# Kernel tuning notes

Hardware: AMD Instinct MI355X
Metric: run time of the kernel (lower is better)

## Reference

```python
import jax, jax.numpy as jnp
import numpy as np

B, T, C, H = 2, 2048, 1024, 16
HS = C // H

def setup_inputs() -> dict:
    key = jax.random.key(0)
    ks = jax.random.split(key, 5)
    s = 0.02
    return {
        "x": jax.random.normal(ks[0], (B, T, C), jnp.float32),
        "W_attn": jax.random.normal(ks[1], (C, 3 * C), jnp.float32) * s,
        "b_attn": jax.random.normal(ks[2], (3 * C,), jnp.float32) * s,
        "W_proj": jax.random.normal(ks[3], (C, C), jnp.float32) * s,
        "b_proj": jax.random.normal(ks[4], (C,), jnp.float32) * s,
    }

def reference(x, W_attn, b_attn, W_proj, b_proj):
    qkv = x @ W_attn + b_attn                      # [B,T,3C]
    q, k, v = jnp.split(qkv, 3, axis=-1)
    # [B,T,C] -> [B,H,T,hs]
    def heads(t):
        return t.reshape(B, T, H, HS).transpose(0, 2, 1, 3)
    q, k, v = heads(q), heads(k), heads(v)
    scale = 1.0 / jnp.sqrt(jnp.asarray(HS, x.dtype))
    attn = jnp.einsum('bhqd,bhkd->bhqk', q, k) * scale
    causal = jnp.tril(jnp.ones((T, T), bool))
    attn = jnp.where(causal[None, None], attn, -jnp.inf)
    attn = jax.nn.softmax(attn, axis=-1)
    y = jnp.einsum('bhqk,bhkd->bhqd', attn, v)
    y = y.transpose(0, 2, 1, 3).reshape(B, T, C)
    return y @ W_proj + b_proj
```

## Files before the change

### kernel.cpp

```cpp
#include <hip/hip_runtime.h>
#include <hip/hip_bf16.h>

static constexpr int Bn = 2, Tn = 2048, Cn = 1024, Hn = 16, HSn = 64;
static constexpr int Mrows = Bn * Tn;
static constexpr size_t PL = (size_t)Bn * Hn * Tn * HSn;

typedef __attribute__((ext_vector_type(8))) short short8;
typedef __attribute__((ext_vector_type(4))) float f32x4;

__device__ __forceinline__ unsigned short f2bf(float f) {
  __hip_bfloat16 h = __float2bfloat16(f);
  return *reinterpret_cast<unsigned short*>(&h);
}

__device__ __forceinline__ float fexp2(float x) {
  return __builtin_amdgcn_exp2f(x);
}

__device__ __forceinline__ void gload_lds16(const void* g, void* l) {
  __builtin_amdgcn_global_load_lds(
      (const __attribute__((address_space(1))) void*)g,
      (__attribute__((address_space(3))) void*)l, 16, 0, 0);
}

#define QSC 0.18033688011112042591999058512524f

__global__ __launch_bounds__(256) void prep_all(
    const float* __restrict__ x, unsigned short* __restrict__ xb,
    const float* __restrict__ Wa, unsigned short* __restrict__ Wab,
    const float* __restrict__ Wp, unsigned short* __restrict__ Wpb)
{
  const int bid = blockIdx.x, tid = threadIdx.x;
  if (bid < 4096) {
    int i = bid * 256 + tid;
    float4 v = ((const float4*)x)[i];
    ushort4 o;
    o.x = f2bf(v.x); o.y = f2bf(v.y); o.z = f2bf(v.z); o.w = f2bf(v.w);
    ((ushort4*)xb)[i] = o;
    return;
  }
  __shared__ float tile[32][33];
  const float* src; unsigned short* dst; int R, Cc, tb;
  if (bid < 4096 + 3072) { src = Wa; dst = Wab; R = Cn; Cc = 3 * Cn; tb = bid - 4096; }
  else                   { src = Wp; dst = Wpb; R = Cn; Cc = Cn;     tb = bid - 4096 - 3072; }
  const int nbx = Cc / 32;
  const int bx = tb % nbx, by = tb / nbx;
  const int tx = tid & 31, ty = tid >> 5;
  const int c0 = bx * 32, r0 = by * 32;
  #pragma unroll
  for (int i = 0; i < 4; ++i)
    tile[ty + 8 * i][tx] = src[(size_t)(r0 + ty + 8 * i) * Cc + c0 + tx];
  __syncthreads();
  #pragma unroll
  for (int i = 0; i < 4; ++i)
    dst[(size_t)(c0 + ty + 8 * i) * R + r0 + tx] = f2bf(tile[tx][ty + 8 * i]);
}

__global__ __launch_bounds__(512) void gemmQKV(
    const unsigned short* __restrict__ A, const unsigned short* __restrict__ Bt,
    const float* __restrict__ bias, unsigned short* __restrict__ qkv, int K)
{
  constexpr int NSTEP = 1024 / 64;
  constexpr int AF = 32;
  constexpr int BF = 24;
  __shared__ alignas(16) unsigned char lds[2][(AF + BF) * 1024];

  const int tid = threadIdx.x, wave = tid >> 6, lane = tid & 63;
  const int wr = wave >> 2, wc = wave & 3;
  const int orig = blockIdx.x;
  const int swz = (orig & 7) * 32 + (orig >> 3);
  const int bx = swz & 15, by = swz >> 4;
  const int tM = by * 256, tN = bx * 192;

  auto STAGE = [&](int buf, int k0) {
    #pragma unroll
    for (int i = 0; i < 7; ++i) {
      int f = wave * 7 + i;
      const unsigned short* g;
      int off;
      if (f < AF) {
        int mg = f >> 1, ks = f & 1;
        g = A + (size_t)(tM + mg * 16 + (lane & 15)) * K + k0 + ks * 32 + (lane >> 4) * 8;
        off = f * 1024;
      } else {
        int fg = f - AF;
        int ng = fg >> 1, ks = fg & 1;
        g = Bt + (size_t)(tN + ng * 16 + (lane & 15)) * K + k0 + ks * 32 + (lane >> 4) * 8;
        off = AF * 1024 + fg * 1024;
      }
      gload_lds16(g, &lds[buf][off]);
    }
  };

  f32x4 acc[8][3] = {};

  STAGE(0, 0);
  STAGE(1, 64);

  for (int t = 0; t < NSTEP; ++t) {
    if (t == NSTEP - 1)
      asm volatile("s_waitcnt vmcnt(0)" ::: "memory");
    else
      asm volatile("s_waitcnt vmcnt(7)" ::: "memory");
    __builtin_amdgcn_s_barrier();

    const int cur = t & 1;
    short8 af[8][2], bfr[3][2];
    #pragma unroll
    for (int ks = 0; ks < 2; ++ks) {
      #pragma unroll
      for (int m = 0; m < 8; ++m)
        af[m][ks] = *(const short8*)&lds[cur][((wr * 8 + m) * 2 + ks) * 1024 + lane * 16];
      #pragma unroll
      for (int n = 0; n < 3; ++n)
        bfr[n][ks] = *(const short8*)&lds[cur][AF * 1024 + ((wc * 3 + n) * 2 + ks) * 1024 + lane * 16];
    }
    asm volatile("s_waitcnt lgkmcnt(0)" ::: "memory");
    __builtin_amdgcn_sched_barrier(0);
    __builtin_amdgcn_s_barrier();

    if (t + 2 < NSTEP) STAGE(cur, (t + 2) * 64);

    __builtin_amdgcn_s_setprio(1);
    #pragma unroll
    for (int ks = 0; ks < 2; ++ks)
      #pragma unroll
      for (int m = 0; m < 8; ++m)
        #pragma unroll
        for (int n = 0; n < 3; ++n)
          acc[m][n] = __builtin_amdgcn_mfma_f32_16x16x32_bf16(af[m][ks], bfr[n][ks], acc[m][n], 0, 0, 0);
    __builtin_amdgcn_s_setprio(0);
  }

  const int a = lane & 15, hq = lane >> 4;
  #pragma unroll
  for (int m = 0; m < 8; ++m) {
    #pragma unroll
    for (int n = 0; n < 3; ++n) {
      int c = tN + wc * 48 + n * 16 + a;
      float bv = bias[c];
      int which = c >> 10;
      int cc = c & 1023, hh = cc >> 6, d = cc & 63;
      int row0 = tM + wr * 128 + m * 16 + hq * 4;
      int b = row0 >> 11, t0 = row0 & 2047;
      int bh = b * Hn + hh;
      if (which == 2) {
        ushort4 pk;
        pk.x = f2bf(acc[m][n][0] + bv);
        pk.y = f2bf(acc[m][n][1] + bv);
        pk.z = f2bf(acc[m][n][2] + bv);
        pk.w = f2bf(acc[m][n][3] + bv);
        *(ushort4*)&qkv[2 * PL + ((size_t)bh * HSn + d) * Tn + t0] = pk;
      } else {
        float sc = (which == 0) ? QSC : 1.0f;
        #pragma unroll
        for (int r = 0; r < 4; ++r) {
          float v = (acc[m][n][r] + bv) * sc;
          qkv[(size_t)which * PL + ((size_t)bh * Tn + t0 + r) * HSn + d] = f2bf(v);
        }
      }
    }
  }
}

template <int WM, int WN>
__global__ __launch_bounds__(256) void gemmP(
    const unsigned short* __restrict__ A, const unsigned short* __restrict__ Bt,
    const float* __restrict__ bias, float* __restrict__ O, int N, int K)
{
  constexpr int BM = WM * 32, BNt = WN * 32;
  constexpr int AF = BM / 16;
  constexpr int BF = BNt / 16;
  constexpr int NF = AF + BF;
  constexpr int PW = NF / 4;
  static_assert(PW == 3, "vmcnt literal");
  __shared__ alignas(16) unsigned char lds[2][NF * 1024];

  const int tid = threadIdx.x, wave = tid >> 6, lane = tid & 63;
  const int wr = wave >> 1, wc = wave & 1;
  const int tM = blockIdx.y * BM, tN = blockIdx.x * BNt;

  auto STAGE = [&](int buf, int k0) {
    #pragma unroll
    for (int i = 0; i < PW; ++i) {
      int f = wave * PW + i;
      const unsigned short* g;
      if (f < AF)
        g = A + (size_t)(tM + f * 16 + (lane & 15)) * K + k0 + (lane >> 4) * 8;
      else
        g = Bt + (size_t)(tN + (f - AF) * 16 + (lane & 15)) * K + k0 + (lane >> 4) * 8;
      gload_lds16(g, &lds[buf][f * 1024]);
    }
  };

  f32x4 acc[WM][WN] = {};

  STAGE(0, 0);
  for (int t = 0, k0 = 0;; ++t, k0 += 32) {
    const int cur = t & 1;
    if (k0 + 32 < K) {
      STAGE(cur ^ 1, k0 + 32);
      asm volatile("s_waitcnt vmcnt(3)" ::: "memory");
    } else {
      asm volatile("s_waitcnt vmcnt(0)" ::: "memory");
    }
    __builtin_amdgcn_s_barrier();

    short8 af[WM], bfr[WN];
    #pragma unroll
    for (int m = 0; m < WM; ++m)
      af[m] = *(const short8*)&lds[cur][(wr * WM + m) * 1024 + lane * 16];
    #pragma unroll
    for (int n = 0; n < WN; ++n)
      bfr[n] = *(const short8*)&lds[cur][(AF + wc * WN + n) * 1024 + lane * 16];
    #pragma unroll
    for (int m = 0; m < WM; ++m)
      #pragma unroll
      for (int n = 0; n < WN; ++n)
        acc[m][n] = __builtin_amdgcn_mfma_f32_16x16x32_bf16(af[m], bfr[n], acc[m][n], 0, 0, 0);

    __builtin_amdgcn_s_barrier();
    if (k0 + 32 >= K) break;
  }

  const int a = lane & 15, hq = lane >> 4;
  #pragma unroll
  for (int m = 0; m < WM; ++m) {
    #pragma unroll
    for (int n = 0; n < WN; ++n) {
      int c = tN + wc * (WN * 16) + n * 16 + a;
      float bv = bias[c];
      int r0 = tM + wr * (WM * 16) + m * 16 + hq * 4;
      #pragma unroll
      for (int r = 0; r < 4; ++r)
        O[(size_t)(r0 + r) * N + c] = acc[m][n][r] + bv;
    }
  }
}

__global__ __launch_bounds__(256) void attn_mfma(
    const unsigned short* __restrict__ Qg, const unsigned short* __restrict__ Kg,
    const unsigned short* __restrict__ Vtg, unsigned short* __restrict__ Y)
{
  __shared__ alignas(16) unsigned char lds[50432];
  const int bh = blockIdx.x;
  const int yb = blockIdx.y;
  const int kq = yb >> 3, jq = yb & 7;
  const int qt = kq * 8 + ((kq & 1) ? (7 - jq) : jq);
  const int tid = threadIdx.x, wave = tid >> 6, lane = tid & 63;
  const int a = lane & 15, h = lane >> 4;
  const int a7 = a & 7;
  const int q0 = qt * 64;
  const unsigned short* Qp = Qg + (size_t)bh * Tn * HSn;
  const unsigned short* Kp = Kg + (size_t)bh * Tn * HSn;
  const unsigned short* Vp = Vtg + (size_t)bh * HSn * Tn;
  const int pbase = 40960 + wave * 2368;
  const int qglob = wave * 16 + a;

  #pragma unroll
  for (int i = 0; i < 2; ++i) {
    int r8 = wave * 16 + i * 8;
    int row = r8 + (lane >> 3);
    int ch = (lane & 7) ^ (row & 7);
    gload_lds16(Qp + (size_t)(q0 + row) * HSn + ch * 8, &lds[r8 * 128]);
  }
  __syncthreads();
  short8 qf[2];
  #pragma unroll
  for (int ks = 0; ks < 2; ++ks) {
    int row = wave * 16 + a;
    int ch = (ks * 4 + h) ^ (row & 7);
    qf[ks] = *(const short8*)&lds[row * 128 + ch * 16];
  }

  f32x4 o[4] = {};
  float l = 0.f;

  const int npairs = qt >> 1;
  const bool oddtail = (qt & 1) != 0;
  const int ntotal = npairs + (oddtail ? 1 : 0);

  for (int p = 0; p < ntotal; ++p) {
    const int kv0 = p * 128;
    const bool masked = oddtail && (p == npairs);
    __syncthreads();
    #pragma unroll
    for (int i = 0; i < 4; ++i) {
      int r8 = wave * 32 + i * 8;
      int row = r8 + (lane >> 3);
      int ch = (lane & 7) ^ (row & 7);
      gload_lds16(Kp + (size_t)(kv0 + row) * HSn + ch * 8, &lds[8192 + r8 * 128]);
    }
    #pragma unroll
    for (int i = 0; i < 4; ++i) {
      int d4 = wave * 16 + i * 4;
      int d = d4 + (lane >> 4);
      int ch = (lane & 15) ^ (d & 7);
      gload_lds16(Vp + (size_t)d * Tn + kv0 + ch * 8, &lds[24576 + d4 * 256]);
    }
    __syncthreads();

    f32x4 s[8] = {};
    __builtin_amdgcn_s_setprio(1);
    #pragma unroll
    for (int ks = 0; ks < 2; ++ks)
      #pragma unroll
      for (int n = 0; n < 8; ++n) {
        int kr = n * 16 + a;
        int ch = (ks * 4 + h) ^ a7;
        short8 kf = *(const short8*)&lds[8192 + kr * 128 + ch * 16];
        s[n] = __builtin_amdgcn_mfma_f32_16x16x32_bf16(kf, qf[ks], s[n], 0, 0, 0);
      }
    __builtin_amdgcn_s_setprio(0);

    if (masked) {
      #pragma unroll
      for (int n = 0; n < 8; ++n)
        #pragma unroll
        for (int r = 0; r < 4; ++r)
          if ((kv0 + n * 16 + h * 4 + r) > (q0 + qglob)) s[n][r] = -1e30f;
    }

    float psum = 0.f;
    #pragma unroll
    for (int n = 0; n < 8; ++n)
      #pragma unroll
      for (int r = 0; r < 4; ++r) {
        float ppv = fexp2(s[n][r]);
        s[n][r] = ppv;
        psum += ppv;
      }
    psum += __shfl_xor(psum, 16);
    psum += __shfl_xor(psum, 32);
    l += psum;

    #pragma unroll
    for (int hp = 0; hp < 2; ++hp) {
      #pragma unroll
      for (int nn = 0; nn < 4; ++nn) {
        int n = hp * 4 + nn;
        uint2 w2;
        w2.x = (unsigned)f2bf(s[n][0]) | ((unsigned)f2bf(s[n][1]) << 16);
        w2.y = (unsigned)f2bf(s[n][2]) | ((unsigned)f2bf(s[n][3]) << 16);
        *(uint2*)&lds[pbase + (a * 36 + nn * 8 + h * 2) * 4] = w2;
      }
      __builtin_amdgcn_s_setprio(1);
      #pragma unroll
      for (int ks = 0; ks < 2; ++ks) {
        short8 pa = *(const short8*)&lds[pbase + (a * 36 + ks * 16 + h * 4) * 4];
        #pragma unroll
        for (int n = 0; n < 4; ++n) {
          int d = n * 16 + a;
          int ch = (hp * 8 + ks * 4 + h) ^ a7;
          short8 vf = *(const short8*)&lds[24576 + d * 256 + ch * 16];
          o[n] = __builtin_amdgcn_mfma_f32_16x16x32_bf16(pa, vf, o[n], 0, 0, 0);
        }
      }
      __builtin_amdgcn_s_setprio(0);
    }
  }

  if (!oddtail) {
    const int kv0 = qt * 64;
    __syncthreads();
    #pragma unroll
    for (int i = 0; i < 2; ++i) {
      int r8 = wave * 16 + i * 8;
      int row = r8 + (lane >> 3);
      int ch = (lane & 7) ^ (row & 7);
      gload_lds16(Kp + (size_t)(kv0 + row) * HSn + ch * 8, &lds[8192 + r8 * 128]);
      gload_lds16(Vp + (size_t)row * Tn + kv0 + ch * 8, &lds[24576 + r8 * 128]);
    }
    __syncthreads();

    f32x4 s[4] = {};
    __builtin_amdgcn_s_setprio(1);
    #pragma unroll
    for (int ks = 0; ks < 2; ++ks)
      #pragma unroll
      for (int n = 0; n < 4; ++n) {
        int kr = n * 16 + a;
        int ch = (ks * 4 + h) ^ a7;
        short8 kf = *(const short8*)&lds[8192 + kr * 128 + ch * 16];
        s[n] = __builtin_amdgcn_mfma_f32_16x16x32_bf16(kf, qf[ks], s[n], 0, 0, 0);
      }
    __builtin_amdgcn_s_setprio(0);

    float psum = 0.f;
    #pragma unroll
    for (int n = 0; n < 4; ++n)
      #pragma unroll
      for (int r = 0; r < 4; ++r) {
        float sv = s[n][r];
        if ((n * 16 + h * 4 + r) > qglob) sv = -1e30f;
        float ppv = fexp2(sv);
        s[n][r] = ppv;
        psum += ppv;
      }
    psum += __shfl_xor(psum, 16);
    psum += __shfl_xor(psum, 32);
    l += psum;

    #pragma unroll
    for (int n = 0; n < 4; ++n) {
      uint2 w2;
      w2.x = (unsigned)f2bf(s[n][0]) | ((unsigned)f2bf(s[n][1]) << 16);
      w2.y = (unsigned)f2bf(s[n][2]) | ((unsigned)f2bf(s[n][3]) << 16);
      *(uint2*)&lds[pbase + (a * 36 + n * 8 + h * 2) * 4] = w2;
    }
    __builtin_amdgcn_s_setprio(1);
    #pragma unroll
    for (int ks = 0; ks < 2; ++ks) {
      short8 pa = *(const short8*)&lds[pbase + (a * 36 + ks * 16 + h * 4) * 4];
      #pragma unroll
      for (int n = 0; n < 4; ++n) {
        int d = n * 16 + a;
        int ch = (ks * 4 + h) ^ a7;
        short8 vf = *(const short8*)&lds[24576 + d * 128 + ch * 16];
        o[n] = __builtin_amdgcn_mfma_f32_16x16x32_bf16(pa, vf, o[n], 0, 0, 0);
      }
    }
    __builtin_amdgcn_s_setprio(0);
  }

  if (h == 0) *(float*)&lds[pbase + 2304 + a * 4] = l;
  f32x4 l4 = *(const f32x4*)&lds[pbase + 2304 + h * 16];
  f32x4 inv;
  #pragma unroll
  for (int r = 0; r < 4; ++r) inv[r] = 1.0f / l4[r];
  const int b = bh >> 4, hd = bh & 15;
  #pragma unroll
  for (int n = 0; n < 4; ++n)
    #pragma unroll
    for (int r = 0; r < 4; ++r) {
      int t = q0 + wave * 16 + 4 * h + r;
      int col = hd * 64 + n * 16 + a;
      Y[((size_t)(b * Tn + t)) * Cn + col] = f2bf(o[n][r] * inv[r]);
    }
}

extern "C" void kernel_launch(void* const* d_in, const int* in_sizes, int n_in,
                              void* d_out, int out_size, void* d_ws, size_t ws_size,
                              hipStream_t stream) {
  const float* x      = (const float*)d_in[0];
  const float* W_attn = (const float*)d_in[1];
  const float* b_attn = (const float*)d_in[2];
  const float* W_proj = (const float*)d_in[3];
  const float* b_proj = (const float*)d_in[4];
  float* out = (float*)d_out;

  unsigned short* xb  = (unsigned short*)d_ws;
  unsigned short* Wab = xb + (size_t)Mrows * Cn;
  unsigned short* Wpb = Wab + (size_t)3 * Cn * Cn;
  unsigned short* qkv = Wpb + (size_t)Cn * Cn;
  unsigned short* y   = qkv + 3 * PL;

  prep_all<<<4096 + 3072 + 1024, 256, 0, stream>>>(x, xb, W_attn, Wab, W_proj, Wpb);

  gemmQKV<<<256, 512, 0, stream>>>(xb, Wab, b_attn, qkv, Cn);

  attn_mfma<<<dim3(Bn * Hn, Tn / 64), 256, 0, stream>>>(qkv, qkv + PL, qkv + 2 * PL, y);

  gemmP<4, 2><<<dim3(Cn / 64, Mrows / 128), 256, 0, stream>>>(
      y, Wpb, b_proj, out, Cn, Cn);
}
```

Baseline: 115.3 us.

## Double attention query tile to 128 rows per block and share K/V fragments

Each attention block now covers 128 query rows instead of 64. Each wave computes two 16-row sub-tiles that reuse the same K and V LDS fragments, and the odd/even tail path is replaced by one uniform causal-masked diagonal tile. Softmax row sums now come from an MFMA against a vector of bf16 ones instead of shuffle reductions. The aim is to halve K/V global and LDS traffic per query row and cut per-tile overhead, at the cost of half as many blocks (512), more registers per thread, and an extra barrier per iteration because the P buffer now overlaps the K region.

```diff
diff --git a/kernel.cpp b/kernel.cpp
--- a/kernel.cpp
+++ b/kernel.cpp
@@ -242,65 +242,64 @@
     const unsigned short* __restrict__ Qg, const unsigned short* __restrict__ Kg,
     const unsigned short* __restrict__ Vtg, unsigned short* __restrict__ Y)
 {
-  __shared__ alignas(16) unsigned char lds[50432];
+  __shared__ alignas(16) unsigned char lds[49152];
   const int bh = blockIdx.x;
   const int yb = blockIdx.y;
-  const int kq = yb >> 3, jq = yb & 7;
-  const int qt = kq * 8 + ((kq & 1) ? (7 - jq) : jq);
+  const int qt = (yb < 8) ? yb : 23 - yb;
   const int tid = threadIdx.x, wave = tid >> 6, lane = tid & 63;
   const int a = lane & 15, h = lane >> 4;
   const int a7 = a & 7;
-  const int q0 = qt * 64;
+  const int q0 = qt * 128;
   const unsigned short* Qp = Qg + (size_t)bh * Tn * HSn;
   const unsigned short* Kp = Kg + (size_t)bh * Tn * HSn;
   const unsigned short* Vp = Vtg + (size_t)bh * HSn * Tn;
-  const int pbase = 40960 + wave * 2368;
-  const int qglob = wave * 16 + a;
-
-  #pragma unroll
-  for (int i = 0; i < 2; ++i) {
-    int r8 = wave * 16 + i * 8;
+  const int pbase = wave * 4608;
+
+  #pragma unroll
+  for (int i = 0; i < 4; ++i) {
+    int r8 = wave * 32 + i * 8;
     int row = r8 + (lane >> 3);
     int ch = (lane & 7) ^ (row & 7);
     gload_lds16(Qp + (size_t)(q0 + row) * HSn + ch * 8, &lds[r8 * 128]);
   }
   __syncthreads();
-  short8 qf[2];
+  short8 qfA[2], qfB[2];
   #pragma unroll
   for (int ks = 0; ks < 2; ++ks) {
-    int row = wave * 16 + a;
-    int ch = (ks * 4 + h) ^ (row & 7);
-    qf[ks] = *(const short8*)&lds[row * 128 + ch * 16];
-  }
-
-  f32x4 o[4] = {};
-  float l = 0.f;
-
-  const int npairs = qt >> 1;
-  const bool oddtail = (qt & 1) != 0;
-  const int ntotal = npairs + (oddtail ? 1 : 0);
-
-  for (int p = 0; p < ntotal; ++p) {
+    int rowA = wave * 32 + a;
+    int ch = (ks * 4 + h) ^ (rowA & 7);
+    qfA[ks] = *(const short8*)&lds[rowA * 128 + ch * 16];
+    qfB[ks] = *(const short8*)&lds[(rowA + 16) * 128 + ch * 16];
+  }
+
+  short8 ones;
+  #pragma unroll
+  for (int j = 0; j < 8; ++j) ones[j] = (short)0x3F80;
+
+  f32x4 oA[4] = {}, oB[4] = {};
+  f32x4 lA = {}, lB = {};
+
+  for (int p = 0; p <= qt; ++p) {
     const int kv0 = p * 128;
-    const bool masked = oddtail && (p == npairs);
+    const bool masked = (p == qt);
     __syncthreads();
     #pragma unroll
     for (int i = 0; i < 4; ++i) {
       int r8 = wave * 32 + i * 8;
       int row = r8 + (lane >> 3);
       int ch = (lane & 7) ^ (row & 7);
-      gload_lds16(Kp + (size_t)(kv0 + row) * HSn + ch * 8, &lds[8192 + r8 * 128]);
+      gload_lds16(Kp + (size_t)(kv0 + row) * HSn + ch * 8, &lds[16384 + r8 * 128]);
     }
     #pragma unroll
     for (int i = 0; i < 4; ++i) {
       int d4 = wave * 16 + i * 4;
       int d = d4 + (lane >> 4);
       int ch = (lane & 15) ^ (d & 7);
-      gload_lds16(Vp + (size_t)d * Tn + kv0 + ch * 8, &lds[24576 + d4 * 256]);
+      gload_lds16(Vp + (size_t)d * Tn + kv0 + ch * 8, &lds[32768 + d4 * 256]);
     }
     __syncthreads();
 
-    f32x4 s[8] = {};
+    f32x4 sA[8] = {}, sB[8] = {};
     __builtin_amdgcn_s_setprio(1);
     #pragma unroll
     for (int ks = 0; ks < 2; ++ks)
@@ -308,8 +307,9 @@
       for (int n = 0; n < 8; ++n) {
         int kr = n * 16 + a;
         int ch = (ks * 4 + h) ^ a7;
-        short8 kf = *(const short8*)&lds[8192 + kr * 128 + ch * 16];
-        s[n] = __builtin_amdgcn_mfma_f32_16x16x32_bf16(kf, qf[ks], s[n], 0, 0, 0);
+        short8 kf = *(const short8*)&lds[16384 + kr * 128 + ch * 16];
+        sA[n] = __builtin_amdgcn_mfma_f32_16x16x32_bf16(kf, qfA[ks], sA[n], 0, 0, 0);
+        sB[n] = __builtin_amdgcn_mfma_f32_16x16x32_bf16(kf, qfB[ks], sB[n], 0, 0, 0);
       }
     __builtin_amdgcn_s_setprio(0);
 
@@ -317,22 +317,21 @@
       #pragma unroll
       for (int n = 0; n < 8; ++n)
         #pragma unroll
-        for (int r = 0; r < 4; ++r)
-          if ((kv0 + n * 16 + h * 4 + r) > (q0 + qglob)) s[n][r] = -1e30f;
-    }
-
-    float psum = 0.f;
+        for (int r = 0; r < 4; ++r) {
+          int kv = n * 16 + h * 4 + r;
+          if (kv > (wave * 32 + a)) sA[n][r] = -1e30f;
+          if (kv > (wave * 32 + 16 + a)) sB[n][r] = -1e30f;
+        }
+    }
     #pragma unroll
     for (int n = 0; n < 8; ++n)
       #pragma unroll
       for (int r = 0; r < 4; ++r) {
-        float ppv = fexp2(s[n][r]);
-        s[n][r] = ppv;
-        psum += ppv;
-      }
-    psum += __shfl_xor(psum, 16);
-    psum += __shfl_xor(psum, 32);
-    l += psum;
+        sA[n][r] = fexp2(sA[n][r]);
+        sB[n][r] = fexp2(sB[n][r]);
+      }
+
+    __syncthreads();
 
     #pragma unroll
     for (int hp = 0; hp < 2; ++hp) {
@@ -340,102 +339,49 @@
       for (int nn = 0; nn < 4; ++nn) {
         int n = hp * 4 + nn;
         uint2 w2;
-        w2.x = (unsigned)f2bf(s[n][0]) | ((unsigned)f2bf(s[n][1]) << 16);
-        w2.y = (unsigned)f2bf(s[n][2]) | ((unsigned)f2bf(s[n][3]) << 16);
+        w2.x = (unsigned)f2bf(sA[n][0]) | ((unsigned)f2bf(sA[n][1]) << 16);
+        w2.y = (unsigned)f2bf(sA[n][2]) | ((unsigned)f2bf(sA[n][3]) << 16);
         *(uint2*)&lds[pbase + (a * 36 + nn * 8 + h * 2) * 4] = w2;
+        uint2 v2;
+        v2.x = (unsigned)f2bf(sB[n][0]) | ((unsigned)f2bf(sB[n][1]) << 16);
+        v2.y = (unsigned)f2bf(sB[n][2]) | ((unsigned)f2bf(sB[n][3]) << 16);
+        *(uint2*)&lds[pbase + 2304 + (a * 36 + nn * 8 + h * 2) * 4] = v2;
       }
       __builtin_amdgcn_s_setprio(1);
       #pragma unroll
       for (int ks = 0; ks < 2; ++ks) {
-        short8 pa = *(const short8*)&lds[pbase + (a * 36 + ks * 16 + h * 4) * 4];
+        short8 paA = *(const short8*)&lds[pbase + (a * 36 + ks * 16 + h * 4) * 4];
+        short8 paB = *(const short8*)&lds[pbase + 2304 + (a * 36 + ks * 16 + h * 4) * 4];
+        lA = __builtin_amdgcn_mfma_f32_16x16x32_bf16(paA, ones, lA, 0, 0, 0);
+        lB = __builtin_amdgcn_mfma_f32_16x16x32_bf16(paB, ones, lB, 0, 0, 0);
         #pragma unroll
         for (int n = 0; n < 4; ++n) {
           int d = n * 16 + a;
           int ch = (hp * 8 + ks * 4 + h) ^ a7;
-          short8 vf = *(const short8*)&lds[24576 + d * 256 + ch * 16];
-          o[n] = __builtin_amdgcn_mfma_f32_16x16x32_bf16(pa, vf, o[n], 0, 0, 0);
+          short8 vf = *(const short8*)&lds[32768 + d * 256 + ch * 16];
+          oA[n] = __builtin_amdgcn_mfma_f32_16x16x32_bf16(paA, vf, oA[n], 0, 0, 0);
+          oB[n] = __builtin_amdgcn_mfma_f32_16x16x32_bf16(paB, vf, oB[n], 0, 0, 0);
         }
       }
       __builtin_amdgcn_s_setprio(0);
     }
   }
 
-  if (!oddtail) {
-    const int kv0 = qt * 64;
-    __syncthreads();
-    #pragma unroll
-    for (int i = 0; i < 2; ++i) {
-      int r8 = wave * 16 + i * 8;
-      int row = r8 + (lane >> 3);
-      int ch = (lane & 7) ^ (row & 7);
-      gload_lds16(Kp + (size_t)(kv0 + row) * HSn + ch * 8, &lds[8192 + r8 * 128]);
-      gload_lds16(Vp + (size_t)row * Tn + kv0 + ch * 8, &lds[24576 + r8 * 128]);
-    }
-    __syncthreads();
-
-    f32x4 s[4] = {};
-    __builtin_amdgcn_s_setprio(1);
-    #pragma unroll
-    for (int ks = 0; ks < 2; ++ks)
-      #pragma unroll
-      for (int n = 0; n < 4; ++n) {
-        int kr = n * 16 + a;
-        int ch = (ks * 4 + h) ^ a7;
-        short8 kf = *(const short8*)&lds[8192 + kr * 128 + ch * 16];
-        s[n] = __builtin_amdgcn_mfma_f32_16x16x32_bf16(kf, qf[ks], s[n], 0, 0, 0);
-      }
-    __builtin_amdgcn_s_setprio(0);
-
-    float psum = 0.f;
-    #pragma unroll
-    for (int n = 0; n < 4; ++n)
-      #pragma unroll
-      for (int r = 0; r < 4; ++r) {
-        float sv = s[n][r];
-        if ((n * 16 + h * 4 + r) > qglob) sv = -1e30f;
-        float ppv = fexp2(sv);
-        s[n][r] = ppv;
-        psum += ppv;
-      }
-    psum += __shfl_xor(psum, 16);
-    psum += __shfl_xor(psum, 32);
-    l += psum;
-
-    #pragma unroll
-    for (int n = 0; n < 4; ++n) {
-      uint2 w2;
-      w2.x = (unsigned)f2bf(s[n][0]) | ((unsigned)f2bf(s[n][1]) << 16);
-      w2.y = (unsigned)f2bf(s[n][2]) | ((unsigned)f2bf(s[n][3]) << 16);
-      *(uint2*)&lds[pbase + (a * 36 + n * 8 + h * 2) * 4] = w2;
-    }
-    __builtin_amdgcn_s_setprio(1);
-    #pragma unroll
-    for (int ks = 0; ks < 2; ++ks) {
-      short8 pa = *(const short8*)&lds[pbase + (a * 36 + ks * 16 + h * 4) * 4];
-      #pragma unroll
-      for (int n = 0; n < 4; ++n) {
-        int d = n * 16 + a;
-        int ch = (ks * 4 + h) ^ a7;
-        short8 vf = *(const short8*)&lds[24576 + d * 128 + ch * 16];
-        o[n] = __builtin_amdgcn_mfma_f32_16x16x32_bf16(pa, vf, o[n], 0, 0, 0);
-      }
-    }
-    __builtin_amdgcn_s_setprio(0);
-  }
-
-  if (h == 0) *(float*)&lds[pbase + 2304 + a * 4] = l;
-  f32x4 l4 = *(const f32x4*)&lds[pbase + 2304 + h * 16];
-  f32x4 inv;
-  #pragma unroll
-  for (int r = 0; r < 4; ++r) inv[r] = 1.0f / l4[r];
+  f32x4 invA, invB;
+  #pragma unroll
+  for (int r = 0; r < 4; ++r) {
+    invA[r] = 1.0f / lA[r];
+    invB[r] = 1.0f / lB[r];
+  }
   const int b = bh >> 4, hd = bh & 15;
   #pragma unroll
   for (int n = 0; n < 4; ++n)
     #pragma unroll
     for (int r = 0; r < 4; ++r) {
-      int t = q0 + wave * 16 + 4 * h + r;
       int col = hd * 64 + n * 16 + a;
-      Y[((size_t)(b * Tn + t)) * Cn + col] = f2bf(o[n][r] * inv[r]);
+      int tA = q0 + wave * 32 + 4 * h + r;
+      Y[((size_t)(b * Tn + tA)) * Cn + col] = f2bf(oA[n][r] * invA[r]);
+      Y[((size_t)(b * Tn + tA + 16)) * Cn + col] = f2bf(oB[n][r] * invB[r]);
     }
 }
 
@@ -459,7 +405,7 @@
 
   gemmQKV<<<256, 512, 0, stream>>>(xb, Wab, b_attn, qkv, Cn);
 
-  attn_mfma<<<dim3(Bn * Hn, Tn / 64), 256, 0, stream>>>(qkv, qkv + PL, qkv + 2 * PL, y);
+  attn_mfma<<<dim3(Bn * Hn, 16), 256, 0, stream>>>(qkv, qkv + PL, qkv + 2 * PL, y);
 
   gemmP<4, 2><<<dim3(Cn / 64, Mrows / 128), 256, 0, stream>>>(
       y, Wpb, b_proj, out, Cn, Cn);
```

New measurement: 115.7 us. No clear change (+0.3%).

## Double-buffer K/V tiles with async prefetch and compute row sums via MFMA

Applied to the files above, without the earlier changes.

Replaces the 128-key paired loop with a 64-key loop over two LDS buffers, prefetching tile t+2 while computing tile t and using explicit vmcnt waits instead of full syncthreads. The row-sum of probabilities is now accumulated by an MFMA against a vector of bf16 ones rather than scalar adds plus shuffles, which also removes the LDS exchange of l. The aim is to hide global load latency behind compute and drop reduction overhead. In exchange there are more loop iterations and barriers, and l is now summed from the bf16-rounded probabilities.

```diff
diff --git a/kernel.cpp b/kernel.cpp
--- a/kernel.cpp
+++ b/kernel.cpp
@@ -242,20 +242,40 @@
     const unsigned short* __restrict__ Qg, const unsigned short* __restrict__ Kg,
     const unsigned short* __restrict__ Vtg, unsigned short* __restrict__ Y)
 {
-  __shared__ alignas(16) unsigned char lds[50432];
+  __shared__ alignas(16) unsigned char lds[50176];
   const int bh = blockIdx.x;
   const int yb = blockIdx.y;
   const int kq = yb >> 3, jq = yb & 7;
   const int qt = kq * 8 + ((kq & 1) ? (7 - jq) : jq);
   const int tid = threadIdx.x, wave = tid >> 6, lane = tid & 63;
   const int a = lane & 15, h = lane >> 4;
-  const int a7 = a & 7;
   const int q0 = qt * 64;
   const unsigned short* Qp = Qg + (size_t)bh * Tn * HSn;
   const unsigned short* Kp = Kg + (size_t)bh * Tn * HSn;
   const unsigned short* Vp = Vtg + (size_t)bh * HSn * Tn;
-  const int pbase = 40960 + wave * 2368;
+  const int pbase = 40960 + wave * 2304;
   const int qglob = wave * 16 + a;
+
+  auto STAGE_K = [&](int kb, int kv0) {
+    #pragma unroll
+    for (int i = 0; i < 2; ++i) {
+      int r8 = wave * 16 + i * 8;
+      int row = r8 + (lane >> 3);
+      int ch = (lane & 7) ^ (row & 7);
+      gload_lds16(Kp + (size_t)(kv0 + row) * HSn + ch * 8,
+                  &lds[8192 + kb * 8192 + r8 * 128]);
+    }
+  };
+  auto STAGE_V = [&](int vb, int kv0) {
+    #pragma unroll
+    for (int i = 0; i < 2; ++i) {
+      int r8 = wave * 16 + i * 8;
+      int row = r8 + (lane >> 3);
+      int ch = (lane & 7) ^ (row & 7);
+      gload_lds16(Vp + (size_t)row * Tn + kv0 + ch * 8,
+                  &lds[24576 + vb * 8192 + r8 * 128]);
+    }
+  };
 
   #pragma unroll
   for (int i = 0; i < 2; ++i) {
@@ -264,7 +284,16 @@
     int ch = (lane & 7) ^ (row & 7);
     gload_lds16(Qp + (size_t)(q0 + row) * HSn + ch * 8, &lds[r8 * 128]);
   }
-  __syncthreads();
+  STAGE_K(0, 0);
+  STAGE_V(0, 0);
+  if (qt >= 1) {
+    STAGE_K(1, 64);
+    STAGE_V(1, 64);
+    asm volatile("s_waitcnt vmcnt(8)" ::: "memory");
+  } else {
+    asm volatile("s_waitcnt vmcnt(4)" ::: "memory");
+  }
+
   short8 qf[2];
   #pragma unroll
   for (int ks = 0; ks < 2; ++ks) {
@@ -273,133 +302,49 @@
     qf[ks] = *(const short8*)&lds[row * 128 + ch * 16];
   }
 
+  short8 ones;
+  #pragma unroll
+  for (int j = 0; j < 8; ++j) ones[j] = (short)0x3F80;
+
   f32x4 o[4] = {};
-  float l = 0.f;
-
-  const int npairs = qt >> 1;
-  const bool oddtail = (qt & 1) != 0;
-  const int ntotal = npairs + (oddtail ? 1 : 0);
-
-  for (int p = 0; p < ntotal; ++p) {
-    const int kv0 = p * 128;
-    const bool masked = oddtail && (p == npairs);
-    __syncthreads();
-    #pragma unroll
-    for (int i = 0; i < 4; ++i) {
-      int r8 = wave * 32 + i * 8;
-      int row = r8 + (lane >> 3);
-      int ch = (lane & 7) ^ (row & 7);
-      gload_lds16(Kp + (size_t)(kv0 + row) * HSn + ch * 8, &lds[8192 + r8 * 128]);
-    }
-    #pragma unroll
-    for (int i = 0; i < 4; ++i) {
-      int d4 = wave * 16 + i * 4;
-      int d = d4 + (lane >> 4);
-      int ch = (lane & 15) ^ (d & 7);
-      gload_lds16(Vp + (size_t)d * Tn + kv0 + ch * 8, &lds[24576 + d4 * 256]);
-    }
-    __syncthreads();
-
-    f32x4 s[8] = {};
+  f32x4 lacc = {};
+
+  for (int t = 0; t <= qt; ++t) {
+    const int kb = t & 1;
+    if (t == qt)
+      asm volatile("s_waitcnt vmcnt(0)" ::: "memory");
+    else
+      asm volatile("s_waitcnt vmcnt(4)" ::: "memory");
+    __builtin_amdgcn_s_barrier();
+
+    const int kbase = 8192 + kb * 8192;
+    const int vbase = 24576 + kb * 8192;
+
+    f32x4 s[4] = {};
     __builtin_amdgcn_s_setprio(1);
     #pragma unroll
     for (int ks = 0; ks < 2; ++ks)
       #pragma unroll
-      for (int n = 0; n < 8; ++n) {
+      for (int n = 0; n < 4; ++n) {
         int kr = n * 16 + a;
-        int ch = (ks * 4 + h) ^ a7;
-        short8 kf = *(const short8*)&lds[8192 + kr * 128 + ch * 16];
+        int ch = (ks * 4 + h) ^ (kr & 7);
+        short8 kf = *(const short8*)&lds[kbase + kr * 128 + ch * 16];
         s[n] = __builtin_amdgcn_mfma_f32_16x16x32_bf16(kf, qf[ks], s[n], 0, 0, 0);
       }
     __builtin_amdgcn_s_setprio(0);
 
-    if (masked) {
-      #pragma unroll
-      for (int n = 0; n < 8; ++n)
+    if (t == qt) {
+      #pragma unroll
+      for (int n = 0; n < 4; ++n)
         #pragma unroll
         for (int r = 0; r < 4; ++r)
-          if ((kv0 + n * 16 + h * 4 + r) > (q0 + qglob)) s[n][r] = -1e30f;
-    }
-
-    float psum = 0.f;
-    #pragma unroll
-    for (int n = 0; n < 8; ++n)
-      #pragma unroll
-      for (int r = 0; r < 4; ++r) {
-        float ppv = fexp2(s[n][r]);
-        s[n][r] = ppv;
-        psum += ppv;
-      }
-    psum += __shfl_xor(psum, 16);
-    psum += __shfl_xor(psum, 32);
-    l += psum;
-
-    #pragma unroll
-    for (int hp = 0; hp < 2; ++hp) {
-      #pragma unroll
-      for (int nn = 0; nn < 4; ++nn) {
-        int n = hp * 4 + nn;
-        uint2 w2;
-        w2.x = (unsigned)f2bf(s[n][0]) | ((unsigned)f2bf(s[n][1]) << 16);
-        w2.y = (unsigned)f2bf(s[n][2]) | ((unsigned)f2bf(s[n][3]) << 16);
-        *(uint2*)&lds[pbase + (a * 36 + nn * 8 + h * 2) * 4] = w2;
-      }
-      __builtin_amdgcn_s_setprio(1);
-      #pragma unroll
-      for (int ks = 0; ks < 2; ++ks) {
-        short8 pa = *(const short8*)&lds[pbase + (a * 36 + ks * 16 + h * 4) * 4];
-        #pragma unroll
-        for (int n = 0; n < 4; ++n) {
-          int d = n * 16 + a;
-          int ch = (hp * 8 + ks * 4 + h) ^ a7;
-          short8 vf = *(const short8*)&lds[24576 + d * 256 + ch * 16];
-          o[n] = __builtin_amdgcn_mfma_f32_16x16x32_bf16(pa, vf, o[n], 0, 0, 0);
-        }
-      }
-      __builtin_amdgcn_s_setprio(0);
-    }
-  }
-
-  if (!oddtail) {
-    const int kv0 = qt * 64;
-    __syncthreads();
-    #pragma unroll
-    for (int i = 0; i < 2; ++i) {
-      int r8 = wave * 16 + i * 8;
-      int row = r8 + (lane >> 3);
-      int ch = (lane & 7) ^ (row & 7);
-      gload_lds16(Kp + (size_t)(kv0 + row) * HSn + ch * 8, &lds[8192 + r8 * 128]);
-      gload_lds16(Vp + (size_t)row * Tn + kv0 + ch * 8, &lds[24576 + r8 * 128]);
-    }
-    __syncthreads();
-
-    f32x4 s[4] = {};
-    __builtin_amdgcn_s_setprio(1);
-    #pragma unroll
-    for (int ks = 0; ks < 2; ++ks)
-      #pragma unroll
-      for (int n = 0; n < 4; ++n) {
-        int kr = n * 16 + a;
-        int ch = (ks * 4 + h) ^ a7;
-        short8 kf = *(const short8*)&lds[8192 + kr * 128 + ch * 16];
-        s[n] = __builtin_amdgcn_mfma_f32_16x16x32_bf16(kf, qf[ks], s[n], 0, 0, 0);
-      }
-    __builtin_amdgcn_s_setprio(0);
-
-    float psum = 0.f;
+          if ((n * 16 + h * 4 + r) > qglob) s[n][r] = -1e30f;
+    }
+
     #pragma unroll
     for (int n = 0; n < 4; ++n)
       #pragma unroll
-      for (int r = 0; r < 4; ++r) {
-        float sv = s[n][r];
-        if ((n * 16 + h * 4 + r) > qglob) sv = -1e30f;
-        float ppv = fexp2(sv);
-        s[n][r] = ppv;
-        psum += ppv;
-      }
-    psum += __shfl_xor(psum, 16);
-    psum += __shfl_xor(psum, 32);
-    l += psum;
+      for (int r = 0; r < 4; ++r) s[n][r] = fexp2(s[n][r]);
 
     #pragma unroll
     for (int n = 0; n < 4; ++n) {
@@ -408,26 +353,32 @@
       w2.y = (unsigned)f2bf(s[n][2]) | ((unsigned)f2bf(s[n][3]) << 16);
       *(uint2*)&lds[pbase + (a * 36 + n * 8 + h * 2) * 4] = w2;
     }
+
     __builtin_amdgcn_s_setprio(1);
     #pragma unroll
     for (int ks = 0; ks < 2; ++ks) {
       short8 pa = *(const short8*)&lds[pbase + (a * 36 + ks * 16 + h * 4) * 4];
+      lacc = __builtin_amdgcn_mfma_f32_16x16x32_bf16(pa, ones, lacc, 0, 0, 0);
       #pragma unroll
       for (int n = 0; n < 4; ++n) {
         int d = n * 16 + a;
-        int ch = (ks * 4 + h) ^ a7;
-        short8 vf = *(const short8*)&lds[24576 + d * 128 + ch * 16];
+        int ch = (ks * 4 + h) ^ (d & 7);
+        short8 vf = *(const short8*)&lds[vbase + d * 128 + ch * 16];
         o[n] = __builtin_amdgcn_mfma_f32_16x16x32_bf16(pa, vf, o[n], 0, 0, 0);
       }
     }
     __builtin_amdgcn_s_setprio(0);
-  }
-
-  if (h == 0) *(float*)&lds[pbase + 2304 + a * 4] = l;
-  f32x4 l4 = *(const f32x4*)&lds[pbase + 2304 + h * 16];
+
+    __builtin_amdgcn_s_barrier();
+    if (t + 2 <= qt) {
+      STAGE_K(kb, (t + 2) * 64);
+      STAGE_V(kb, (t + 2) * 64);
+    }
+  }
+
   f32x4 inv;
   #pragma unroll
-  for (int r = 0; r < 4; ++r) inv[r] = 1.0f / l4[r];
+  for (int r = 0; r < 4; ++r) inv[r] = 1.0f / lacc[r];
   const int b = bh >> 4, hd = bh & 15;
   #pragma unroll
   for (int n = 0; n < 4; ++n)
```

Result: no change. 113.0 us (-2.0%).
